# Kernel optimization log

Measured on AMD Instinct MI355X. Metric: run time of the kernel, lower is better.

The kernel has to match this reference:

```python
import jax, jax.numpy as jnp
import numpy as np

B, N, D = 16, 1024, 1152
H = 16; DH = D // H
GH = GW = 32; SY = SX = 2
WS = SY * SX                      # tokens per window
NW = (GH // SY) * (GW // SX)      # 256 windows (one dst each)
NS = NW * (WS - 1)                # 768 src tokens
NUM_PRUNE = int(N * 0.5)          # 512
NOISE_ALPHA = 0.1
SIM_BETA = 1.0


def setup_inputs() -> dict:
    key = jax.random.key(0)
    ks = jax.random.split(key, 8)
    rn = lambda k, s: jax.random.normal(k, s, jnp.float32) * 0.02
    return dict(
        x=jax.random.normal(ks[0], (B, N, D), jnp.float32),
        noise=jax.random.uniform(ks[1], (B, NW, WS), jnp.float32),
        ln1_g=jnp.ones((D,), jnp.float32), ln1_b=jnp.zeros((D,), jnp.float32),
        ln2_g=jnp.ones((D,), jnp.float32), ln2_b=jnp.zeros((D,), jnp.float32),
        w_qkv=rn(ks[2], (D, 3 * D)), b_qkv=jnp.zeros((3 * D,), jnp.float32),
        w_proj=rn(ks[3], (D, D)), b_proj=jnp.zeros((D,), jnp.float32),
        w_fc1=rn(ks[4], (D, 4 * D)), b_fc1=jnp.zeros((4 * D,), jnp.float32),
        w_fc2=rn(ks[5], (4 * D, D)), b_fc2=jnp.zeros((D,), jnp.float32),
    )


def _ln(x, g, b):
    mu = x.mean(-1, keepdims=True)
    var = ((x - mu) ** 2).mean(-1, keepdims=True)
    return (x - mu) * jax.lax.rsqrt(var + 1e-6) * g + b


def _dit_block(x, ln1_g, ln1_b, ln2_g, ln2_b, w_qkv, b_qkv, w_proj, b_proj,
               w_fc1, b_fc1, w_fc2, b_fc2):
    Bq, T, _ = x.shape
    y = _ln(x, ln1_g, ln1_b)
    q, k, v = jnp.split(y @ w_qkv + b_qkv, 3, axis=-1)
    hd = lambda t: t.reshape(Bq, T, H, DH).transpose(0, 2, 1, 3)  # [B,H,T,DH]
    q, k, v = hd(q), hd(k), hd(v)
    att = jax.nn.softmax(jnp.einsum('bhqd,bhkd->bhqk', q, k) * (1.0 / np.sqrt(DH)), axis=-1)
    o = jnp.einsum('bhqk,bhkd->bhqd', att, v).transpose(0, 2, 1, 3).reshape(Bq, T, D)
    x = x + o @ w_proj + b_proj
    y = _ln(x, ln2_g, ln2_b)
    return x + jax.nn.gelu(y @ w_fc1 + b_fc1) @ w_fc2 + b_fc2


def _sito_indices(x, noise):
    # SiTo seed (dst) selection + similarity-based prune index computation.
    xn = x / (jnp.linalg.norm(x, axis=-1, keepdims=True) + 1e-6)  # cosine feats
    grid = jnp.arange(N).reshape(GH, GW)
    win = grid.reshape(GH // SY, SY, GW // SX, SX).transpose(0, 2, 1, 3).reshape(NW, WS)
    xw = xn[:, win]                                   # [B,NW,WS,D]
    mean = xw.mean(2, keepdims=True)
    score = SIM_BETA * (xw * mean).sum(-1) + NOISE_ALPHA * noise  # [B,NW,WS]
    dst_local = jnp.argmax(score, axis=-1)            # [B,NW]
    winb = jnp.broadcast_to(win, (B, NW, WS))
    dst_idx = jnp.take_along_axis(winb, dst_local[..., None], -1)[..., 0]  # [B,NW]
    local = jnp.arange(WS)[None, None]
    keymat = jnp.where(local != dst_local[..., None], local, WS)
    src_local = jnp.sort(keymat, -1)[..., : WS - 1]   # non-dst locals, in order
    src_idx = jnp.take_along_axis(winb, src_local, -1).reshape(B, NS)
    a = jnp.take_along_axis(xn, src_idx[..., None], 1)      # [B,NS,D]
    bf = jnp.take_along_axis(xn, dst_idx[..., None], 1)     # [B,NW,D]
    sim = jnp.einsum('bsd,bnd->bsn', a, bf)                 # [B,NS,NW]
    best = jnp.argmax(sim, -1)                              # most-similar dst
    order = jnp.argsort(-jnp.max(sim, -1), axis=-1)
    pruned_pos = order[:, :NUM_PRUNE]
    kept_pos = order[:, NUM_PRUNE:]
    src_kept = jnp.take_along_axis(src_idx, kept_pos, 1)
    src_pruned = jnp.take_along_axis(src_idx, pruned_pos, 1)
    pruned_best = jnp.take_along_axis(best, pruned_pos, 1)
    return dst_idx, src_kept, src_pruned, pruned_best


def reference(x, noise, ln1_g, ln1_b, ln2_g, ln2_b, w_qkv, b_qkv, w_proj, b_proj,
              w_fc1, b_fc1, w_fc2, b_fc2):
    dst_idx, src_kept, src_pruned, pruned_best = _sito_indices(x, noise)
    keep_idx = jnp.concatenate([dst_idx, src_kept], axis=1)          # [B,Nk]
    xk = jnp.take_along_axis(x, keep_idx[..., None], 1)              # prune_fn
    out = _dit_block(xk, ln1_g, ln1_b, ln2_g, ln2_b, w_qkv, b_qkv,
                     w_proj, b_proj, w_fc1, b_fc1, w_fc2, b_fc2)

    def recover_one(o, di, sk, sp, pb):  # recover_fn: scatter + copy-from-dst
        out_dst, out_src = o[:NW], o[NW:]
        full = jnp.zeros((N, D), o.dtype)
        full = full.at[di].set(out_dst)
        full = full.at[sk].set(out_src)
        return full.at[sp].set(out_dst[pb])

    return jax.vmap(recover_one)(out, dst_idx, src_kept, src_pruned, pruned_best)
```

## Files before the change

### kernel.cpp

```cpp
#include <hip/hip_runtime.h>
#include <hip/hip_bf16.h>

namespace {

constexpr int Dd = 1152;

typedef __attribute__((ext_vector_type(8))) short bf16x8;
typedef __attribute__((ext_vector_type(4))) float f32x4;

__device__ __forceinline__ void gload_lds16(const void* g, void* l) {
  __builtin_amdgcn_global_load_lds(
      (const __attribute__((address_space(1))) void*)g,
      (__attribute__((address_space(3))) void*)l, 16, 0, 0);
}

__device__ __forceinline__ float gelu_f(float x) {
  float x3 = x * x * x;
  float z2 = 1.5957691216057308f * (x + 0.044715f * x3);
  float e = __expf(fminf(z2, 30.0f));
  return x * e / (e + 1.0f);
}

__global__ __launch_bounds__(256) void norm_kernel(const float* __restrict__ x,
    float* __restrict__ inv, __hip_bfloat16* __restrict__ xnh,
    __hip_bfloat16* __restrict__ xnl) {
  int row = blockIdx.x * 4 + (threadIdx.x >> 6);
  int lane = threadIdx.x & 63;
  const float2* xr = (const float2*)(x + (size_t)row * Dd);
  float2 v[9];
  float s = 0.f;
  #pragma unroll
  for (int e = 0; e < 9; ++e) {
    v[e] = xr[lane + 64 * e];
    s += v[e].x * v[e].x + v[e].y * v[e].y;
  }
  #pragma unroll
  for (int m = 1; m < 64; m <<= 1) s += __shfl_xor(s, m);
  float iv = 1.0f / (sqrtf(s) + 1e-6f);
  if (lane == 0) inv[row] = iv;
  ushort2* ph = (ushort2*)(xnh + (size_t)row * Dd);
  ushort2* pl = (ushort2*)(xnl + (size_t)row * Dd);
  #pragma unroll
  for (int e = 0; e < 9; ++e) {
    float ax = v[e].x * iv, ay = v[e].y * iv;
    __hip_bfloat16 hx = __float2bfloat16(ax), hy = __float2bfloat16(ay);
    __hip_bfloat16 lx = __float2bfloat16(ax - __bfloat162float(hx));
    __hip_bfloat16 ly = __float2bfloat16(ay - __bfloat162float(hy));
    ph[lane + 64 * e] = make_ushort2(*(ushort*)&hx, *(ushort*)&hy);
    pl[lane + 64 * e] = make_ushort2(*(ushort*)&lx, *(ushort*)&ly);
  }
}

__global__ __launch_bounds__(256) void window_kernel(const float* __restrict__ x,
    const float* __restrict__ inv, const float* __restrict__ noise,
    int* __restrict__ dsti, int* __restrict__ srci) {
  int gidx = blockIdx.x * 4 + (threadIdx.x >> 6);
  int lane = threadIdx.x & 63;
  int b = gidx >> 8, w = gidx & 255;
  int wy = w >> 4, wx = w & 15;
  int t0 = (wy * 2) * 32 + wx * 2;
  int tk[4] = {t0, t0 + 1, t0 + 32, t0 + 33};
  float iv[4]; const float* xr[4];
  #pragma unroll
  for (int j = 0; j < 4; ++j) {
    iv[j] = inv[b * 1024 + tk[j]];
    xr[j] = x + (size_t)(b * 1024 + tk[j]) * Dd;
  }
  float dot[4] = {0.f, 0.f, 0.f, 0.f};
  for (int d = lane; d < Dd; d += 64) {
    float xn[4], sum = 0.f;
    #pragma unroll
    for (int j = 0; j < 4; ++j) { xn[j] = xr[j][d] * iv[j]; sum += xn[j]; }
    #pragma unroll
    for (int j = 0; j < 4; ++j) dot[j] += xn[j] * sum;
  }
  #pragma unroll
  for (int m = 1; m < 64; m <<= 1)
    #pragma unroll
    for (int j = 0; j < 4; ++j) dot[j] += __shfl_xor(dot[j], m);
  if (lane == 0) {
    float best = -1e30f; int bj = 0;
    #pragma unroll
    for (int j = 0; j < 4; ++j) {
      float sc = 0.25f * dot[j] + 0.1f * noise[(size_t)(b * 256 + w) * 4 + j];
      if (sc > best) { best = sc; bj = j; }
    }
    dsti[b * 256 + w] = tk[bj];
    int m = 0;
    #pragma unroll
    for (int j = 0; j < 4; ++j) if (j != bj) srci[b * 768 + w * 3 + (m++)] = tk[j];
  }
}

__global__ __launch_bounds__(256) void simgemm_kernel(
    const __hip_bfloat16* __restrict__ xnh, const __hip_bfloat16* __restrict__ xnl,
    const int* __restrict__ dsti, const int* __restrict__ srci,
    float* __restrict__ mx, int* __restrict__ best) {
  int b = blockIdx.x / 12;
  int m0 = (blockIdx.x % 12) * 64;
  __shared__ __align__(16) __hip_bfloat16 AsH[2][64 * 32];
  __shared__ __align__(16) __hip_bfloat16 AsL[2][64 * 32];
  __shared__ __align__(16) __hip_bfloat16 BsH[2][256 * 32];
  __shared__ __align__(16) __hip_bfloat16 BsL[2][256 * 32];
  const int tid = threadIdx.x, wid = tid >> 6, lane = tid & 63;
  const int g = lane >> 4, lr = lane & 15;

  const int slotRow = tid >> 2;
  const int colByte = (((tid & 3) ^ ((tid >> 3) & 3)) << 4);
  size_t aRow = (size_t)((b << 10) + srci[b * 768 + m0 + slotRow]) * Dd;
  size_t bRow[4];
  #pragma unroll
  for (int p = 0; p < 4; ++p)
    bRow[p] = (size_t)((b << 10) + dsti[b * 256 + p * 64 + slotRow]) * Dd;
  const char* xh = (const char*)xnh;
  const char* xl = (const char*)xnl;

  auto stage = [&](int buf, int k0) {
    size_t ka = (aRow + k0) * 2 + colByte;
    gload_lds16(xh + ka, (char*)AsH + buf * 4096 + wid * 1024);
    gload_lds16(xl + ka, (char*)AsL + buf * 4096 + wid * 1024);
    #pragma unroll
    for (int p = 0; p < 4; ++p) {
      size_t kb = (bRow[p] + k0) * 2 + colByte;
      gload_lds16(xh + kb, (char*)BsH + buf * 16384 + p * 4096 + wid * 1024);
      gload_lds16(xl + kb, (char*)BsL + buf * 16384 + p * 4096 + wid * 1024);
    }
  };

  f32x4 hh[16], hx[16];
  const f32x4 zf = {0.f, 0.f, 0.f, 0.f};
  #pragma unroll
  for (int nf = 0; nf < 16; ++nf) { hh[nf] = zf; hx[nf] = zf; }

  const int roff = ((g ^ ((lr >> 1) & 3)) << 3);
  stage(0, 0);
  asm volatile("s_waitcnt vmcnt(0)" ::: "memory");
  __syncthreads();
  int buf = 0;
  for (int ks = 0; ks < 36; ++ks) {
    if (ks + 1 < 36) stage(buf ^ 1, (ks + 1) * 32);
    bf16x8 ah = *(const bf16x8*)&AsH[buf][(wid * 16 + lr) * 32 + roff];
    bf16x8 al = *(const bf16x8*)&AsL[buf][(wid * 16 + lr) * 32 + roff];
    #pragma unroll
    for (int nf = 0; nf < 16; ++nf) {
      bf16x8 bh = *(const bf16x8*)&BsH[buf][(nf * 16 + lr) * 32 + roff];
      bf16x8 bl = *(const bf16x8*)&BsL[buf][(nf * 16 + lr) * 32 + roff];
      hh[nf] = __builtin_amdgcn_mfma_f32_16x16x32_bf16(ah, bh, hh[nf], 0, 0, 0);
      hx[nf] = __builtin_amdgcn_mfma_f32_16x16x32_bf16(ah, bl, hx[nf], 0, 0, 0);
      hx[nf] = __builtin_amdgcn_mfma_f32_16x16x32_bf16(al, bh, hx[nf], 0, 0, 0);
    }
    asm volatile("s_waitcnt vmcnt(0)" ::: "memory");
    __syncthreads();
    buf ^= 1;
  }

  #pragma unroll
  for (int j = 0; j < 4; ++j) {
    float bv = -1e30f; int bi = 0;
    #pragma unroll
    for (int nf = 0; nf < 16; ++nf) {
      float v = hh[nf][j] + hx[nf][j];
      if (v > bv) { bv = v; bi = nf * 16 + lr; }
    }
    #pragma unroll
    for (int m = 1; m < 16; m <<= 1) {
      float ov = __shfl_xor(bv, m);
      int oi = __shfl_xor(bi, m);
      if (ov > bv || (ov == bv && oi < bi)) { bv = ov; bi = oi; }
    }
    if (lr == 0) {
      int row = m0 + wid * 16 + g * 4 + j;
      mx[b * 768 + row] = bv;
      best[b * 768 + row] = bi;
    }
  }
}

__global__ __launch_bounds__(256) void rank_kernel(const float* __restrict__ mx,
    const int* __restrict__ best, const int* __restrict__ dsti,
    const int* __restrict__ srci, int* __restrict__ keep, int* __restrict__ srow) {
  int b = blockIdx.x;
  int tid = threadIdx.x;
  __shared__ float smx[768];
  for (int i = tid; i < 768; i += 256) smx[i] = mx[b * 768 + i];
  __syncthreads();
  if (tid < 256) {
    int t = dsti[b * 256 + tid];
    keep[b * 512 + tid] = t;
    srow[b * 1024 + t] = tid;
  }
  for (int i = tid; i < 768; i += 256) {
    float v = smx[i];
    int r = 0;
    for (int s = 0; s < 768; ++s) {
      float u = smx[s];
      r += (u > v) || (u == v && s < i);
    }
    int tok = srci[b * 768 + i];
    if (r >= 512) {
      keep[b * 512 + (r - 256)] = tok;
      srow[b * 1024 + tok] = r - 256;
    } else {
      srow[b * 1024 + tok] = best[b * 768 + i];
    }
  }
}

template<int GATHER>
__global__ __launch_bounds__(256) void ln_kernel(const float* __restrict__ xin,
    const int* __restrict__ keep, const float* __restrict__ gw,
    const float* __restrict__ bw, __hip_bfloat16* __restrict__ yout,
    float* __restrict__ xkout) {
  int row = blockIdx.x;
  const float* xr;
  float* xo = nullptr;
  if (GATHER) {
    int b = row >> 9, t = row & 511;
    int tok = keep[(b << 9) + t];
    xr = xin + (size_t)((b << 10) + tok) * Dd;
    xo = xkout + (size_t)row * Dd;
  } else {
    xr = xin + (size_t)row * Dd;
  }
  int tid = threadIdx.x;
  float v[5];
  float s = 0.f, s2 = 0.f;
  #pragma unroll
  for (int e = 0; e < 5; ++e) {
    int i = tid + e * 256;
    float val = (i < Dd) ? xr[i] : 0.f;
    v[e] = val; s += val; s2 += val * val;
  }
  #pragma unroll
  for (int m = 1; m < 64; m <<= 1) { s += __shfl_xor(s, m); s2 += __shfl_xor(s2, m); }
  __shared__ float ps[4], ps2[4];
  int wid = tid >> 6, lane = tid & 63;
  if (lane == 0) { ps[wid] = s; ps2[wid] = s2; }
  __syncthreads();
  s = ps[0] + ps[1] + ps[2] + ps[3];
  s2 = ps2[0] + ps2[1] + ps2[2] + ps2[3];
  constexpr float inv_d = 1.0f / Dd;
  float mu = s * inv_d;
  float var = s2 * inv_d - mu * mu;
  float rstd = rsqrtf(var + 1e-6f);
  __hip_bfloat16* yr = yout + (size_t)row * Dd;
  #pragma unroll
  for (int e = 0; e < 5; ++e) {
    int i = tid + e * 256;
    if (i < Dd) {
      yr[i] = __float2bfloat16((v[e] - mu) * rstd * gw[i] + bw[i]);
      if (GATHER) xo[i] = v[e];
    }
  }
}

__global__ __launch_bounds__(256) void wtrans_kernel(const float* __restrict__ w,
    __hip_bfloat16* __restrict__ wT, int K, int N) {
  __shared__ float tile[32][33];
  int nt = N >> 5;
  int tk = blockIdx.x / nt, tn = blockIdx.x % nt;
  int tid = threadIdx.x;
  #pragma unroll
  for (int e = 0; e < 4; ++e) {
    int idx = tid + e * 256;
    int r = idx >> 5, c = idx & 31;
    tile[r][c] = w[(size_t)(tk * 32 + r) * N + tn * 32 + c];
  }
  __syncthreads();
  #pragma unroll
  for (int e = 0; e < 4; ++e) {
    int idx = tid + e * 256;
    int r = idx >> 5, c = idx & 31;
    wT[(size_t)(tn * 32 + r) * K + tk * 32 + c] = __float2bfloat16(tile[c][r]);
  }
}

template<int EPI>
__device__ __forceinline__ void epi_store(void* C, const float* res, int Nd,
                                          size_t row, size_t col, float v) {
  if (EPI == 0) {
    ((__hip_bfloat16*)C)[row * (size_t)Nd + col] = __float2bfloat16(v);
  } else if (EPI == 1) {
    ((float*)C)[row * (size_t)Nd + col] = v + res[row * (size_t)Nd + col];
  } else {
    ((__hip_bfloat16*)C)[row * (size_t)Nd + col] = __float2bfloat16(gelu_f(v));
  }
}

template<int EPI, int BMT>
__global__ __launch_bounds__(512, BMT == 1 ? 4 : 2) void gemm256_kernel(
    const __hip_bfloat16* __restrict__ A, const __hip_bfloat16* __restrict__ BT,
    const float* __restrict__ bias, const float* __restrict__ res,
    void* __restrict__ C, int Md, int Nd, int NdPad, int Kd) {
  constexpr int BM = BMT * 128;
  constexpr int MI = BMT * 4;
  constexpr int LL = BMT + 2;
  __shared__ __align__(16) __hip_bfloat16 As[3][BM * 32];
  __shared__ __align__(16) __hip_bfloat16 Bs[3][256 * 32];
  const int nb = NdPad >> 8;
  const int q8 = gridDim.x >> 3;
  const int wg = (blockIdx.x & 7) * q8 + (blockIdx.x >> 3);
  const int bm = wg / nb, bnb = wg % nb;
  const int tid = threadIdx.x, wid = tid >> 6, lane = tid & 63;
  const int g = lane >> 4, lr = lane & 15;
  const int wm = wid >> 2, wn = wid & 3;
  const size_t m0 = (size_t)bm * BM, n0 = (size_t)bnb * 256;

  const int trow = tid >> 2;
  const int scol = (((tid & 3) ^ ((tid >> 3) & 3)) << 3);
  const char* Ab = (const char*)A;
  const char* Bb = (const char*)BT;

  auto stage = [&](int slot, int kt) {
    const size_t kb = ((size_t)kt << 5) + scol;
    #pragma unroll
    for (int c = 0; c < BMT; ++c)
      gload_lds16(Ab + (((m0 + c * 128 + trow) * (size_t)Kd + kb) << 1),
                  (char*)As + slot * (BM * 64) + c * 8192 + wid * 1024);
    #pragma unroll
    for (int c = 0; c < 2; ++c)
      gload_lds16(Bb + (((n0 + c * 128 + trow) * (size_t)Kd + kb) << 1),
                  (char*)Bs + slot * 16384 + c * 8192 + wid * 1024);
  };

  f32x4 acc[MI][4];
  const f32x4 zf = {0.f, 0.f, 0.f, 0.f};
  #pragma unroll
  for (int mi = 0; mi < MI; ++mi)
    #pragma unroll
    for (int ni = 0; ni < 4; ++ni) acc[mi][ni] = zf;

  const int nk = Kd >> 5;
  stage(0, 0);
  stage(1, 1);
  asm volatile("s_waitcnt vmcnt(%0)" :: "i"(LL) : "memory");
  __builtin_amdgcn_s_barrier();

  int cur = 0;
  const int roff = ((g ^ ((lr >> 1) & 3)) << 3);
  for (int kt = 0; kt < nk; ++kt) {
    const __hip_bfloat16* Ac = As[cur];
    const __hip_bfloat16* Bc = Bs[cur];
    bf16x8 af[MI], bf[4];
    #pragma unroll
    for (int mi = 0; mi < MI; ++mi)
      af[mi] = *(const bf16x8*)&Ac[(wm * (BM / 2) + mi * 16 + lr) * 32 + roff];
    #pragma unroll
    for (int ni = 0; ni < 4; ++ni)
      bf[ni] = *(const bf16x8*)&Bc[(wn * 64 + ni * 16 + lr) * 32 + roff];
    if (kt + 2 < nk) stage(cur == 0 ? 2 : cur - 1, kt + 2);
    __builtin_amdgcn_s_barrier();
    __builtin_amdgcn_s_setprio(1);
    #pragma unroll
    for (int mi = 0; mi < MI; ++mi)
      #pragma unroll
      for (int ni = 0; ni < 4; ++ni)
        acc[mi][ni] = __builtin_amdgcn_mfma_f32_16x16x32_bf16(af[mi], bf[ni], acc[mi][ni], 0, 0, 0);
    __builtin_amdgcn_s_setprio(0);
    if (kt + 2 < nk)      asm volatile("s_waitcnt vmcnt(%0)" :: "i"(LL) : "memory");
    else if (kt + 1 < nk) asm volatile("s_waitcnt vmcnt(0)" ::: "memory");
    __builtin_amdgcn_s_barrier();
    cur = (cur == 2) ? 0 : cur + 1;
  }

  #pragma unroll
  for (int ni = 0; ni < 4; ++ni) {
    size_t col = n0 + wn * 64 + ni * 16 + lr;
    if (col < (size_t)Nd) {
      float bv = bias[col];
      #pragma unroll
      for (int mi = 0; mi < MI; ++mi) {
        #pragma unroll
        for (int j = 0; j < 4; ++j) {
          size_t row = m0 + wm * (BM / 2) + mi * 16 + g * 4 + j;
          epi_store<EPI>(C, res, Nd, row, col, acc[mi][ni][j] + bv);
        }
      }
    }
  }
}

__global__ __launch_bounds__(256) void vtrans_kernel(const __hip_bfloat16* __restrict__ qkv,
                                                     __hip_bfloat16* __restrict__ vT) {
  int bh = blockIdx.x;
  int b = bh >> 4, h = bh & 15;
  __shared__ __align__(16) __hip_bfloat16 Vl[256 * 72];
  int tid = threadIdx.x;
  const __hip_bfloat16 zb = __float2bfloat16(0.0f);
  for (int half = 0; half < 2; ++half) {
    __syncthreads();
    for (int idx = tid; idx < 256 * 18; idx += 256) {
      int t = idx / 18, c = idx % 18;
      *(ushort4*)&Vl[t * 72 + c * 4] =
          *(const ushort4*)&qkv[((size_t)(b * 512 + half * 256 + t)) * 3456 + 2304 + h * 72 + c * 4];
    }
    __syncthreads();
    for (int idx = tid; idx < 80 * 256; idx += 256) {
      int d = idx >> 8, t = idx & 255;
      vT[((size_t)bh * 80 + d) * 512 + half * 256 + t] = (d < 72) ? Vl[t * 72 + d] : zb;
    }
  }
}

__global__ __launch_bounds__(256) void attn_kernel(const __hip_bfloat16* __restrict__ qkv,
    const __hip_bfloat16* __restrict__ vT, __hip_bfloat16* __restrict__ o) {
  const int blk = blockIdx.x;
  const int qt = blk & 7, bh = blk >> 3;
  const int b = bh >> 4, h = bh & 15;
  __shared__ __align__(16) __hip_bfloat16 Qs[64][96];
  __shared__ __align__(16) __hip_bfloat16 Ks[64][96];
  __shared__ __align__(16) __hip_bfloat16 Vs[80][72];
  __shared__ __align__(16) __hip_bfloat16 Ps[4][16][72];
  const int tid = threadIdx.x, wid = tid >> 6, lane = tid & 63;
  const int g = lane >> 4, lr = lane & 15;
  const __hip_bfloat16 zb = __float2bfloat16(0.0f);

  for (int idx = tid; idx < 64 * 18; idx += 256) {
    int r = idx / 18, c = idx % 18;
    *(ushort4*)&Qs[r][c * 4] =
        *(const ushort4*)&qkv[((size_t)(b * 512 + qt * 64 + r)) * 3456 + h * 72 + c * 4];
  }
  for (int idx = tid; idx < 64 * 24; idx += 256) {
    int r = idx / 24, d = 72 + idx % 24;
    Qs[r][d] = zb; Ks[r][d] = zb;
  }

  f32x4 ov[5];
  const f32x4 zf = {0.f, 0.f, 0.f, 0.f};
  #pragma unroll
  for (int ni = 0; ni < 5; ++ni) ov[ni] = zf;
  float m_[4], l_[4];
  #pragma unroll
  for (int j = 0; j < 4; ++j) { m_[j] = -3.0e38f; l_[j] = 0.f; }
  const float scale = 0.11785113019775793f;

  for (int c = 0; c < 8; ++c) {
    __syncthreads();
    for (int idx = tid; idx < 64 * 18; idx += 256) {
      int r = idx / 18, cc = idx % 18;
      *(ushort4*)&Ks[r][cc * 4] =
          *(const ushort4*)&qkv[((size_t)(b * 512 + c * 64 + r)) * 3456 + 1152 + h * 72 + cc * 4];
    }
    for (int idx = tid; idx < 80 * 8; idx += 256) {
      int d = idx >> 3, t8 = idx & 7;
      *(uint4*)&Vs[d][t8 * 8] =
          *(const uint4*)&vT[((size_t)bh * 80 + d) * 512 + c * 64 + t8 * 8];
    }
    __syncthreads();

    f32x4 sf[4];
    #pragma unroll
    for (int nf = 0; nf < 4; ++nf) sf[nf] = zf;
    #pragma unroll
    for (int ks = 0; ks < 3; ++ks) {
      bf16x8 qa = *(const bf16x8*)&Qs[wid * 16 + lr][ks * 32 + g * 8];
      #pragma unroll
      for (int nf = 0; nf < 4; ++nf) {
        bf16x8 kb = *(const bf16x8*)&Ks[nf * 16 + lr][ks * 32 + g * 8];
        sf[nf] = __builtin_amdgcn_mfma_f32_16x16x32_bf16(qa, kb, sf[nf], 0, 0, 0);
      }
    }

    float cm[4];
    #pragma unroll
    for (int j = 0; j < 4; ++j)
      cm[j] = fmaxf(fmaxf(sf[0][j], sf[1][j]), fmaxf(sf[2][j], sf[3][j])) * scale;
    #pragma unroll
    for (int mm = 1; mm < 16; mm <<= 1)
      #pragma unroll
      for (int j = 0; j < 4; ++j) cm[j] = fmaxf(cm[j], __shfl_xor(cm[j], mm));
    float fac[4], rs[4];
    #pragma unroll
    for (int j = 0; j < 4; ++j) {
      float nm = fmaxf(m_[j], cm[j]);
      fac[j] = __expf(m_[j] - nm);
      m_[j] = nm;
      rs[j] = 0.f;
    }
    #pragma unroll
    for (int nf = 0; nf < 4; ++nf)
      #pragma unroll
      for (int j = 0; j < 4; ++j) {
        float pv = __expf(sf[nf][j] * scale - m_[j]);
        rs[j] += pv;
        Ps[wid][g * 4 + j][nf * 16 + lr] = __float2bfloat16(pv);
      }
    #pragma unroll
    for (int mm = 1; mm < 16; mm <<= 1)
      #pragma unroll
      for (int j = 0; j < 4; ++j) rs[j] += __shfl_xor(rs[j], mm);
    #pragma unroll
    for (int j = 0; j < 4; ++j) l_[j] = l_[j] * fac[j] + rs[j];
    #pragma unroll
    for (int ni = 0; ni < 5; ++ni)
      #pragma unroll
      for (int j = 0; j < 4; ++j) ov[ni][j] *= fac[j];

    #pragma unroll
    for (int k2 = 0; k2 < 2; ++k2) {
      bf16x8 pa = *(const bf16x8*)&Ps[wid][lr][k2 * 32 + g * 8];
      #pragma unroll
      for (int ni = 0; ni < 5; ++ni) {
        bf16x8 vb = *(const bf16x8*)&Vs[ni * 16 + lr][k2 * 32 + g * 8];
        ov[ni] = __builtin_amdgcn_mfma_f32_16x16x32_bf16(pa, vb, ov[ni], 0, 0, 0);
      }
    }
  }

  #pragma unroll
  for (int ni = 0; ni < 5; ++ni) {
    int d = ni * 16 + lr;
    if (d < 72) {
      #pragma unroll
      for (int j = 0; j < 4; ++j) {
        int t = qt * 64 + wid * 16 + g * 4 + j;
        o[((size_t)(b * 512 + t)) * 1152 + h * 72 + d] = __float2bfloat16(ov[ni][j] / l_[j]);
      }
    }
  }
}

__global__ __launch_bounds__(256) void recover_kernel(const float* __restrict__ yout,
    const int* __restrict__ srow, float* __restrict__ out) {
  int idx = blockIdx.x * 256 + threadIdx.x;
  int q = idx % 288;
  int bnv = idx / 288;
  int r = srow[bnv];
  int b = bnv >> 10;
  const float4* src = (const float4*)yout + ((size_t)((b << 9) + r)) * 288 + q;
  ((float4*)out)[idx] = *src;
}

}

extern "C" void kernel_launch(void* const* d_in, const int* in_sizes, int n_in,
                              void* d_out, int out_size, void* d_ws, size_t ws_size,
                              hipStream_t stream) {
  (void)in_sizes; (void)n_in; (void)out_size; (void)ws_size;
  const float* x      = (const float*)d_in[0];
  const float* noise  = (const float*)d_in[1];
  const float* ln1_g  = (const float*)d_in[2];
  const float* ln1_b  = (const float*)d_in[3];
  const float* ln2_g  = (const float*)d_in[4];
  const float* ln2_b  = (const float*)d_in[5];
  const float* w_qkv  = (const float*)d_in[6];
  const float* b_qkv  = (const float*)d_in[7];
  const float* w_proj = (const float*)d_in[8];
  const float* b_proj = (const float*)d_in[9];
  const float* w_fc1  = (const float*)d_in[10];
  const float* b_fc1  = (const float*)d_in[11];
  const float* w_fc2  = (const float*)d_in[12];
  const float* b_fc2  = (const float*)d_in[13];
  float* out = (float*)d_out;

  char* p = (char*)d_ws;
  auto alloc = [&](size_t bytes) {
    char* r = p;
    p += (bytes + 255) & ~(size_t)255;
    return r;
  };
  __hip_bfloat16* wqkvT  = (__hip_bfloat16*)alloc((size_t)3584 * 1152 * 2);
  __hip_bfloat16* wprojT = (__hip_bfloat16*)alloc((size_t)1280 * 1152 * 2);
  __hip_bfloat16* wfc1T  = (__hip_bfloat16*)alloc((size_t)4608 * 1152 * 2);
  __hip_bfloat16* wfc2T  = (__hip_bfloat16*)alloc((size_t)1280 * 4608 * 2);
  float* inv = (float*)alloc(16384 * 4);
  int* dsti  = (int*)alloc(4096 * 4);
  int* srci  = (int*)alloc(12288 * 4);
  float* mx  = (float*)alloc(12288 * 4);
  int* best  = (int*)alloc(12288 * 4);
  int* keep  = (int*)alloc(8192 * 4);
  int* srow  = (int*)alloc(16384 * 4);
  float* xk  = (float*)alloc((size_t)8192 * 1152 * 4);
  __hip_bfloat16* y1   = (__hip_bfloat16*)alloc((size_t)8192 * 1152 * 2);
  __hip_bfloat16* qkvb = (__hip_bfloat16*)alloc((size_t)8192 * 4608 * 2);
  __hip_bfloat16* vT   = (__hip_bfloat16*)alloc((size_t)256 * 80 * 512 * 2);
  __hip_bfloat16* ob   = (__hip_bfloat16*)alloc((size_t)8192 * 1152 * 2);
  float* x2 = (float*)alloc((size_t)8192 * 1152 * 4);
  float* yout = xk;

  __hip_bfloat16* xnh = qkvb;
  __hip_bfloat16* xnl = qkvb + (size_t)16 * 1024 * 1152;

  wtrans_kernel<<<36 * 108, 256, 0, stream>>>(w_qkv, wqkvT, 1152, 3456);
  wtrans_kernel<<<36 * 36, 256, 0, stream>>>(w_proj, wprojT, 1152, 1152);
  wtrans_kernel<<<36 * 144, 256, 0, stream>>>(w_fc1, wfc1T, 1152, 4608);
  wtrans_kernel<<<144 * 36, 256, 0, stream>>>(w_fc2, wfc2T, 4608, 1152);

  norm_kernel<<<4096, 256, 0, stream>>>(x, inv, xnh, xnl);
  window_kernel<<<1024, 256, 0, stream>>>(x, inv, noise, dsti, srci);
  simgemm_kernel<<<16 * 12, 256, 0, stream>>>(xnh, xnl, dsti, srci, mx, best);
  rank_kernel<<<16, 256, 0, stream>>>(mx, best, dsti, srci, keep, srow);

  ln_kernel<1><<<8192, 256, 0, stream>>>(x, keep, ln1_g, ln1_b, y1, xk);
  gemm256_kernel<0, 2><<<32 * 14, 512, 0, stream>>>(y1, wqkvT, b_qkv, nullptr, qkvb, 8192, 3456, 3584, 1152);
  vtrans_kernel<<<256, 256, 0, stream>>>(qkvb, vT);
  attn_kernel<<<2048, 256, 0, stream>>>(qkvb, vT, ob);
  gemm256_kernel<1, 1><<<64 * 5, 512, 0, stream>>>(ob, wprojT, b_proj, xk, x2, 8192, 1152, 1280, 1152);
  ln_kernel<0><<<8192, 256, 0, stream>>>(x2, nullptr, ln2_g, ln2_b, y1, nullptr);
  gemm256_kernel<2, 2><<<32 * 18, 512, 0, stream>>>(y1, wfc1T, b_fc1, nullptr, qkvb, 8192, 4608, 4608, 1152);
  gemm256_kernel<1, 1><<<64 * 5, 512, 0, stream>>>(qkvb, wfc2T, b_fc2, x2, yout, 8192, 1152, 1280, 4608);

  recover_kernel<<<18432, 256, 0, stream>>>(yout, srow, out);
}
```

Before: 808.0 us.

## Double-buffer LDS fragment reads and prefetch three stages in GEMM main loop

```diff
diff --git a/kernel.cpp b/kernel.cpp
--- a/kernel.cpp
+++ b/kernel.cpp
@@ -288,7 +288,7 @@
 }
 
 template<int EPI, int BMT>
-__global__ __launch_bounds__(512, BMT == 1 ? 4 : 2) void gemm256_kernel(
+__global__ __launch_bounds__(512, 2) void gemmov_kernel(
     const __hip_bfloat16* __restrict__ A, const __hip_bfloat16* __restrict__ BT,
     const float* __restrict__ bias, const float* __restrict__ res,
     void* __restrict__ C, int Md, int Nd, int NdPad, int Kd) {
@@ -330,38 +330,53 @@
     #pragma unroll
     for (int ni = 0; ni < 4; ++ni) acc[mi][ni] = zf;
 
+  const int roff = ((g ^ ((lr >> 1) & 3)) << 3);
   const int nk = Kd >> 5;
-  stage(0, 0);
-  stage(1, 1);
-  asm volatile("s_waitcnt vmcnt(%0)" :: "i"(LL) : "memory");
+
+  bf16x8 afA[MI], bfA[4], afB[MI], bfB[4];
+
+#define DSREAD(AF, BF, SLOT) { \
+  const __hip_bfloat16* Ac_ = As[SLOT]; \
+  const __hip_bfloat16* Bc_ = Bs[SLOT]; \
+  _Pragma("unroll") for (int mi_ = 0; mi_ < MI; ++mi_) \
+    AF[mi_] = *(const bf16x8*)&Ac_[(wm * (BM / 2) + mi_ * 16 + lr) * 32 + roff]; \
+  _Pragma("unroll") for (int ni_ = 0; ni_ < 4; ++ni_) \
+    BF[ni_] = *(const bf16x8*)&Bc_[(wn * 64 + ni_ * 16 + lr) * 32 + roff]; }
+
+#define MFMACL(AF, BF) { \
+  __builtin_amdgcn_s_setprio(1); \
+  _Pragma("unroll") for (int mi_ = 0; mi_ < MI; ++mi_) \
+    _Pragma("unroll") for (int ni_ = 0; ni_ < 4; ++ni_) \
+      acc[mi_][ni_] = __builtin_amdgcn_mfma_f32_16x16x32_bf16(AF[mi_], BF[ni_], acc[mi_][ni_], 0, 0, 0); \
+  __builtin_amdgcn_s_setprio(0); }
+
+#define GITER(KT, S0, S1, AFC, BFC, AFN, BFN) { \
+  if ((KT) <= nk - 3)      { asm volatile("s_waitcnt vmcnt(%0)" :: "i"(LL) : "memory"); } \
+  else if ((KT) == nk - 2) { asm volatile("s_waitcnt vmcnt(0)" ::: "memory"); } \
+  asm volatile("s_waitcnt lgkmcnt(0)" ::: "memory"); \
+  __builtin_amdgcn_s_barrier(); \
+  asm volatile("" ::: "memory"); \
+  if ((KT) + 3 < nk) stage((S0), (KT) + 3); \
+  if ((KT) + 1 < nk) DSREAD(AFN, BFN, (S1)); \
+  __builtin_amdgcn_sched_barrier(0); \
+  MFMACL(AFC, BFC); }
+
+  stage(0, 0); stage(1, 1); stage(2, 2);
+  asm volatile("s_waitcnt vmcnt(%0)" :: "i"(2 * LL) : "memory");
   __builtin_amdgcn_s_barrier();
-
-  int cur = 0;
-  const int roff = ((g ^ ((lr >> 1) & 3)) << 3);
-  for (int kt = 0; kt < nk; ++kt) {
-    const __hip_bfloat16* Ac = As[cur];
-    const __hip_bfloat16* Bc = Bs[cur];
-    bf16x8 af[MI], bf[4];
-    #pragma unroll
-    for (int mi = 0; mi < MI; ++mi)
-      af[mi] = *(const bf16x8*)&Ac[(wm * (BM / 2) + mi * 16 + lr) * 32 + roff];
-    #pragma unroll
-    for (int ni = 0; ni < 4; ++ni)
-      bf[ni] = *(const bf16x8*)&Bc[(wn * 64 + ni * 16 + lr) * 32 + roff];
-    if (kt + 2 < nk) stage(cur == 0 ? 2 : cur - 1, kt + 2);
-    __builtin_amdgcn_s_barrier();
-    __builtin_amdgcn_s_setprio(1);
-    #pragma unroll
-    for (int mi = 0; mi < MI; ++mi)
-      #pragma unroll
-      for (int ni = 0; ni < 4; ++ni)
-        acc[mi][ni] = __builtin_amdgcn_mfma_f32_16x16x32_bf16(af[mi], bf[ni], acc[mi][ni], 0, 0, 0);
-    __builtin_amdgcn_s_setprio(0);
-    if (kt + 2 < nk)      asm volatile("s_waitcnt vmcnt(%0)" :: "i"(LL) : "memory");
-    else if (kt + 1 < nk) asm volatile("s_waitcnt vmcnt(0)" ::: "memory");
-    __builtin_amdgcn_s_barrier();
-    cur = (cur == 2) ? 0 : cur + 1;
-  }
+  asm volatile("" ::: "memory");
+  DSREAD(afA, bfA, 0);
+
+  int s0 = 0, s1 = 1;
+  for (int kt = 0; kt < nk; kt += 2) {
+    GITER(kt, s0, s1, afA, bfA, afB, bfB);
+    int s2 = (s1 == 2) ? 0 : s1 + 1;
+    GITER(kt + 1, s1, s2, afB, bfB, afA, bfA);
+    s0 = s2; s1 = (s2 == 2) ? 0 : s2 + 1;
+  }
+#undef GITER
+#undef MFMACL
+#undef DSREAD
 
   #pragma unroll
   for (int ni = 0; ni < 4; ++ni) {
@@ -592,13 +607,13 @@
   rank_kernel<<<16, 256, 0, stream>>>(mx, best, dsti, srci, keep, srow);
 
   ln_kernel<1><<<8192, 256, 0, stream>>>(x, keep, ln1_g, ln1_b, y1, xk);
-  gemm256_kernel<0, 2><<<32 * 14, 512, 0, stream>>>(y1, wqkvT, b_qkv, nullptr, qkvb, 8192, 3456, 3584, 1152);
+  gemmov_kernel<0, 2><<<32 * 14, 512, 0, stream>>>(y1, wqkvT, b_qkv, nullptr, qkvb, 8192, 3456, 3584, 1152);
   vtrans_kernel<<<256, 256, 0, stream>>>(qkvb, vT);
   attn_kernel<<<2048, 256, 0, stream>>>(qkvb, vT, ob);
-  gemm256_kernel<1, 1><<<64 * 5, 512, 0, stream>>>(ob, wprojT, b_proj, xk, x2, 8192, 1152, 1280, 1152);
+  gemmov_kernel<1, 1><<<64 * 5, 512, 0, stream>>>(ob, wprojT, b_proj, xk, x2, 8192, 1152, 1280, 1152);
   ln_kernel<0><<<8192, 256, 0, stream>>>(x2, nullptr, ln2_g, ln2_b, y1, nullptr);
-  gemm256_kernel<2, 2><<<32 * 18, 512, 0, stream>>>(y1, wfc1T, b_fc1, nullptr, qkvb, 8192, 4608, 4608, 1152);
-  gemm256_kernel<1, 1><<<64 * 5, 512, 0, stream>>>(qkvb, wfc2T, b_fc2, x2, yout, 8192, 1152, 1280, 4608);
+  gemmov_kernel<2, 2><<<32 * 18, 512, 0, stream>>>(y1, wfc1T, b_fc1, nullptr, qkvb, 8192, 4608, 4608, 1152);
+  gemmov_kernel<1, 1><<<64 * 5, 512, 0, stream>>>(qkvb, wfc2T, b_fc2, x2, yout, 8192, 1152, 1280, 4608);
 
   recover_kernel<<<18432, 256, 0, stream>>>(yout, srow, out);
 }
```

Result: slower. 989.4 us (+22.4%).

## Gather residual in proj GEMM epilogue and use 128-row tiles for all GEMMs

Applied to the files above, without the earlier changes.

```diff
diff --git a/kernel.cpp b/kernel.cpp
--- a/kernel.cpp
+++ b/kernel.cpp
@@ -209,16 +209,13 @@
 template<int GATHER>
 __global__ __launch_bounds__(256) void ln_kernel(const float* __restrict__ xin,
     const int* __restrict__ keep, const float* __restrict__ gw,
-    const float* __restrict__ bw, __hip_bfloat16* __restrict__ yout,
-    float* __restrict__ xkout) {
+    const float* __restrict__ bw, __hip_bfloat16* __restrict__ yout) {
   int row = blockIdx.x;
   const float* xr;
-  float* xo = nullptr;
   if (GATHER) {
     int b = row >> 9, t = row & 511;
     int tok = keep[(b << 9) + t];
     xr = xin + (size_t)((b << 10) + tok) * Dd;
-    xo = xkout + (size_t)row * Dd;
   } else {
     xr = xin + (size_t)row * Dd;
   }
@@ -249,7 +246,6 @@
     int i = tid + e * 256;
     if (i < Dd) {
       yr[i] = __float2bfloat16((v[e] - mu) * rstd * gw[i] + bw[i]);
-      if (GATHER) xo[i] = v[e];
     }
   }
 }
@@ -282,19 +278,18 @@
     ((__hip_bfloat16*)C)[row * (size_t)Nd + col] = __float2bfloat16(v);
   } else if (EPI == 1) {
     ((float*)C)[row * (size_t)Nd + col] = v + res[row * (size_t)Nd + col];
-  } else {
+  } else if (EPI == 2) {
     ((__hip_bfloat16*)C)[row * (size_t)Nd + col] = __float2bfloat16(gelu_f(v));
   }
 }
 
-template<int EPI, int BMT>
-__global__ __launch_bounds__(512, BMT == 1 ? 4 : 2) void gemm256_kernel(
+template<int EPI>
+__global__ __launch_bounds__(512, 4) void gemm128_kernel(
     const __hip_bfloat16* __restrict__ A, const __hip_bfloat16* __restrict__ BT,
     const float* __restrict__ bias, const float* __restrict__ res,
+    const int* __restrict__ keepIdx, const float* __restrict__ xsrc,
     void* __restrict__ C, int Md, int Nd, int NdPad, int Kd) {
-  constexpr int BM = BMT * 128;
-  constexpr int MI = BMT * 4;
-  constexpr int LL = BMT + 2;
+  constexpr int BM = 128;
   __shared__ __align__(16) __hip_bfloat16 As[3][BM * 32];
   __shared__ __align__(16) __hip_bfloat16 Bs[3][256 * 32];
   const int nb = NdPad >> 8;
@@ -313,27 +308,25 @@
 
   auto stage = [&](int slot, int kt) {
     const size_t kb = ((size_t)kt << 5) + scol;
-    #pragma unroll
-    for (int c = 0; c < BMT; ++c)
-      gload_lds16(Ab + (((m0 + c * 128 + trow) * (size_t)Kd + kb) << 1),
-                  (char*)As + slot * (BM * 64) + c * 8192 + wid * 1024);
-    #pragma unroll
-    for (int c = 0; c < 2; ++c)
-      gload_lds16(Bb + (((n0 + c * 128 + trow) * (size_t)Kd + kb) << 1),
-                  (char*)Bs + slot * 16384 + c * 8192 + wid * 1024);
+    gload_lds16(Ab + (((m0 + trow) * (size_t)Kd + kb) << 1),
+                (char*)As + slot * 8192 + wid * 1024);
+    gload_lds16(Bb + (((n0 + trow) * (size_t)Kd + kb) << 1),
+                (char*)Bs + slot * 16384 + wid * 1024);
+    gload_lds16(Bb + (((n0 + 128 + trow) * (size_t)Kd + kb) << 1),
+                (char*)Bs + slot * 16384 + 8192 + wid * 1024);
   };
 
-  f32x4 acc[MI][4];
+  f32x4 acc[4][4];
   const f32x4 zf = {0.f, 0.f, 0.f, 0.f};
   #pragma unroll
-  for (int mi = 0; mi < MI; ++mi)
+  for (int mi = 0; mi < 4; ++mi)
     #pragma unroll
     for (int ni = 0; ni < 4; ++ni) acc[mi][ni] = zf;
 
   const int nk = Kd >> 5;
   stage(0, 0);
   stage(1, 1);
-  asm volatile("s_waitcnt vmcnt(%0)" :: "i"(LL) : "memory");
+  asm volatile("s_waitcnt vmcnt(3)" ::: "memory");
   __builtin_amdgcn_s_barrier();
 
   int cur = 0;
@@ -341,10 +334,10 @@
   for (int kt = 0; kt < nk; ++kt) {
     const __hip_bfloat16* Ac = As[cur];
     const __hip_bfloat16* Bc = Bs[cur];
-    bf16x8 af[MI], bf[4];
-    #pragma unroll
-    for (int mi = 0; mi < MI; ++mi)
-      af[mi] = *(const bf16x8*)&Ac[(wm * (BM / 2) + mi * 16 + lr) * 32 + roff];
+    bf16x8 af[4], bf[4];
+    #pragma unroll
+    for (int mi = 0; mi < 4; ++mi)
+      af[mi] = *(const bf16x8*)&Ac[(wm * 64 + mi * 16 + lr) * 32 + roff];
     #pragma unroll
     for (int ni = 0; ni < 4; ++ni)
       bf[ni] = *(const bf16x8*)&Bc[(wn * 64 + ni * 16 + lr) * 32 + roff];
@@ -352,12 +345,12 @@
     __builtin_amdgcn_s_barrier();
     __builtin_amdgcn_s_setprio(1);
     #pragma unroll
-    for (int mi = 0; mi < MI; ++mi)
+    for (int mi = 0; mi < 4; ++mi)
       #pragma unroll
       for (int ni = 0; ni < 4; ++ni)
         acc[mi][ni] = __builtin_amdgcn_mfma_f32_16x16x32_bf16(af[mi], bf[ni], acc[mi][ni], 0, 0, 0);
     __builtin_amdgcn_s_setprio(0);
-    if (kt + 2 < nk)      asm volatile("s_waitcnt vmcnt(%0)" :: "i"(LL) : "memory");
+    if (kt + 2 < nk)      asm volatile("s_waitcnt vmcnt(3)" ::: "memory");
     else if (kt + 1 < nk) asm volatile("s_waitcnt vmcnt(0)" ::: "memory");
     __builtin_amdgcn_s_barrier();
     cur = (cur == 2) ? 0 : cur + 1;
@@ -369,11 +362,19 @@
     if (col < (size_t)Nd) {
       float bv = bias[col];
       #pragma unroll
-      for (int mi = 0; mi < MI; ++mi) {
+      for (int mi = 0; mi < 4; ++mi) {
         #pragma unroll
         for (int j = 0; j < 4; ++j) {
-          size_t row = m0 + wm * (BM / 2) + mi * 16 + g * 4 + j;
-          epi_store<EPI>(C, res, Nd, row, col, acc[mi][ni][j] + bv);
+          size_t row = m0 + wm * 64 + mi * 16 + g * 4 + j;
+          float v = acc[mi][ni][j] + bv;
+          if (EPI == 3) {
+            int b = (int)(row >> 9);
+            int tok = keepIdx[row];
+            const float* rr = xsrc + ((size_t)(b << 10) + tok) * Dd;
+            ((float*)C)[row * (size_t)Nd + col] = v + rr[col];
+          } else {
+            epi_store<EPI>(C, res, Nd, row, col, v);
+          }
         }
       }
     }
@@ -570,13 +571,12 @@
   int* best  = (int*)alloc(12288 * 4);
   int* keep  = (int*)alloc(8192 * 4);
   int* srow  = (int*)alloc(16384 * 4);
-  float* xk  = (float*)alloc((size_t)8192 * 1152 * 4);
+  float* yout = (float*)alloc((size_t)8192 * 1152 * 4);
   __hip_bfloat16* y1   = (__hip_bfloat16*)alloc((size_t)8192 * 1152 * 2);
   __hip_bfloat16* qkvb = (__hip_bfloat16*)alloc((size_t)8192 * 4608 * 2);
   __hip_bfloat16* vT   = (__hip_bfloat16*)alloc((size_t)256 * 80 * 512 * 2);
   __hip_bfloat16* ob   = (__hip_bfloat16*)alloc((size_t)8192 * 1152 * 2);
   float* x2 = (float*)alloc((size_t)8192 * 1152 * 4);
-  float* yout = xk;
 
   __hip_bfloat16* xnh = qkvb;
   __hip_bfloat16* xnl = qkvb + (size_t)16 * 1024 * 1152;
@@ -591,14 +591,18 @@
   simgemm_kernel<<<16 * 12, 256, 0, stream>>>(xnh, xnl, dsti, srci, mx, best);
   rank_kernel<<<16, 256, 0, stream>>>(mx, best, dsti, srci, keep, srow);
 
-  ln_kernel<1><<<8192, 256, 0, stream>>>(x, keep, ln1_g, ln1_b, y1, xk);
-  gemm256_kernel<0, 2><<<32 * 14, 512, 0, stream>>>(y1, wqkvT, b_qkv, nullptr, qkvb, 8192, 3456, 3584, 1152);
+  ln_kernel<1><<<8192, 256, 0, stream>>>(x, keep, ln1_g, ln1_b, y1);
+  gemm128_kernel<0><<<64 * 14, 512, 0, stream>>>(y1, wqkvT, b_qkv, nullptr, nullptr, nullptr,
+                                                 qkvb, 8192, 3456, 3584, 1152);
   vtrans_kernel<<<256, 256, 0, stream>>>(qkvb, vT);
   attn_kernel<<<2048, 256, 0, stream>>>(qkvb, vT, ob);
-  gemm256_kernel<1, 1><<<64 * 5, 512, 0, stream>>>(ob, wprojT, b_proj, xk, x2, 8192, 1152, 1280, 1152);
-  ln_kernel<0><<<8192, 256, 0, stream>>>(x2, nullptr, ln2_g, ln2_b, y1, nullptr);
-  gemm256_kernel<2, 2><<<32 * 18, 512, 0, stream>>>(y1, wfc1T, b_fc1, nullptr, qkvb, 8192, 4608, 4608, 1152);
-  gemm256_kernel<1, 1><<<64 * 5, 512, 0, stream>>>(qkvb, wfc2T, b_fc2, x2, yout, 8192, 1152, 1280, 4608);
+  gemm128_kernel<3><<<64 * 5, 512, 0, stream>>>(ob, wprojT, b_proj, nullptr, keep, x,
+                                                x2, 8192, 1152, 1280, 1152);
+  ln_kernel<0><<<8192, 256, 0, stream>>>(x2, nullptr, ln2_g, ln2_b, y1);
+  gemm128_kernel<2><<<64 * 18, 512, 0, stream>>>(y1, wfc1T, b_fc1, nullptr, nullptr, nullptr,
+                                                 qkvb, 8192, 4608, 4608, 1152);
+  gemm128_kernel<1><<<64 * 5, 512, 0, stream>>>(qkvb, wfc2T, b_fc2, x2, nullptr, nullptr,
+                                                yout, 8192, 1152, 1280, 4608);
 
   recover_kernel<<<18432, 256, 0, stream>>>(yout, srow, out);
 }
```

Measured after the change: 769.4 us. 4.8% less time.
